# Kernel tuning notes

Measured on AMD Instinct MI355X. Metric: run time of the kernel, lower is better.

The kernel has to match this reference:

```python
import jax, jax.numpy as jnp
import numpy as np

V, H_BASE, D, L, K = 32000, 4096, 512, 2, 4
B = 64

def setup_inputs() -> dict:
    key = jax.random.key(0)
    ks = jax.random.split(key, 12)
    s = 0.02
    return {
        "hidden_state": jax.random.normal(ks[0], (B, H_BASE), jnp.float32),
        "in_proj_w": jax.random.normal(ks[1], (D, H_BASE), jnp.float32) * s,
        "in_proj_b": jnp.zeros((D,), jnp.float32),
        "w_ih0": jax.random.normal(ks[2], (3 * D, D), jnp.float32) * s,
        "w_hh0": jax.random.normal(ks[3], (3 * D, D), jnp.float32) * s,
        "b_ih0": jax.random.normal(ks[4], (3 * D,), jnp.float32) * s,
        "b_hh0": jax.random.normal(ks[5], (3 * D,), jnp.float32) * s,
        "w_ih1": jax.random.normal(ks[6], (3 * D, D), jnp.float32) * s,
        "w_hh1": jax.random.normal(ks[7], (3 * D, D), jnp.float32) * s,
        "b_ih1": jax.random.normal(ks[8], (3 * D,), jnp.float32) * s,
        "b_hh1": jax.random.normal(ks[9], (3 * D,), jnp.float32) * s,
        "embed": jax.random.normal(ks[10], (V, D), jnp.float32) * s,
        "out_w": jax.random.normal(ks[11], (V, D), jnp.float32) * s,
    }

def _gru_cell(x, h, w_ih, w_hh, b_ih, b_hh):
    # PyTorch GRU gate order: r, z, n
    gi = x @ w_ih.T + b_ih  # [B, 3D]
    gh = h @ w_hh.T + b_hh
    ir, iz, inn = jnp.split(gi, 3, axis=-1)
    hr, hz, hn = jnp.split(gh, 3, axis=-1)
    r = jax.nn.sigmoid(ir + hr)
    z = jax.nn.sigmoid(iz + hz)
    n = jnp.tanh(inn + r * hn)
    return (1.0 - z) * n + z * h

def reference(hidden_state, in_proj_w, in_proj_b, w_ih0, w_hh0, b_ih0, b_hh0,
              w_ih1, w_hh1, b_ih1, b_hh1, embed, out_w):
    b = hidden_state.shape[0]
    h0 = hidden_state @ in_proj_w.T + in_proj_b  # [B, D]
    h_l0 = h0
    h_l1 = h0
    x = jnp.zeros((b, in_proj_w.shape[0]), hidden_state.dtype)
    all_logits = []
    for _ in range(K):
        h_l0 = _gru_cell(x, h_l0, w_ih0, w_hh0, b_ih0, b_hh0)
        h_l1 = _gru_cell(h_l0, h_l1, w_ih1, w_hh1, b_ih1, b_hh1)
        logits = h_l1 @ out_w.T  # [B, V]
        all_logits.append(logits)
        x = embed[jnp.argmax(logits, axis=-1)]  # greedy next-token embed
    return jnp.stack(all_logits, axis=1)  # [B, K, V]
```

## Files before the change

### kernel.cpp

```cpp
#include <hip/hip_runtime.h>
#include <math.h>


typedef __attribute__((ext_vector_type(8))) short short8;
typedef __attribute__((ext_vector_type(4))) float f32x4;

__device__ __forceinline__ unsigned short f2bf_rne(float x) {
    unsigned u = __float_as_uint(x);
    unsigned r = (u + 0x7fffu + ((u >> 16) & 1u)) >> 16;
    return (unsigned short)r;
}
__device__ __forceinline__ void split2(float x, unsigned short& hi, unsigned short& lo) {
    unsigned u = __float_as_uint(x);
    hi = (unsigned short)(u >> 16);
    float r = x - __uint_as_float(u & 0xffff0000u);
    lo = f2bf_rne(r);
}

__device__ __forceinline__ void store_plane(unsigned short* hiP, unsigned short* loP,
                                            int m, int d, float v) {
    int s = d >> 6, cl = (d >> 3) & 7, e = d & 7;
    int off = m * 512 + s * 64 + ((cl ^ (m & 7)) * 8) + e;
    unsigned short hi, lo; split2(v, hi, lo);
    hiP[off] = hi; loP[off] = lo;
}

__device__ __forceinline__ void gload16(const void* g, void* lds) {
    __builtin_amdgcn_global_load_lds(
        (const __attribute__((address_space(1))) unsigned int*)g,
        (__attribute__((address_space(3))) unsigned int*)lds, 16, 0, 0);
}

__device__ __forceinline__ void split_w_body(
    const float* __restrict__ W, unsigned short* __restrict__ H,
    unsigned short* __restrict__ L, size_t g, int kclog)
{
    int n  = (int)(g >> kclog);
    int c8 = (int)g & ((1 << kclog) - 1);
    const float* src = W + g * 8;
    float4 v0 = *(const float4*)src;
    float4 v1 = *(const float4*)(src + 4);
    unsigned short h[8], l[8];
    split2(v0.x,h[0],l[0]); split2(v0.y,h[1],l[1]); split2(v0.z,h[2],l[2]); split2(v0.w,h[3],l[3]);
    split2(v1.x,h[4],l[4]); split2(v1.y,h[5],l[5]); split2(v1.z,h[6],l[6]); split2(v1.w,h[7],l[7]);
    uint4 ph = make_uint4((unsigned)h[0]|((unsigned)h[1]<<16), (unsigned)h[2]|((unsigned)h[3]<<16),
                          (unsigned)h[4]|((unsigned)h[5]<<16), (unsigned)h[6]|((unsigned)h[7]<<16));
    uint4 pl = make_uint4((unsigned)l[0]|((unsigned)l[1]<<16), (unsigned)l[2]|((unsigned)l[3]<<16),
                          (unsigned)l[4]|((unsigned)l[5]<<16), (unsigned)l[6]|((unsigned)l[7]<<16));
    int nt = n >> 7, row = n & 127;
    int ksi = c8 >> 3;
    int slot = (c8 & 7) ^ (row & 7);
    int tpr = 1 << (kclog - 3);
    size_t off = ((size_t)(nt * tpr + ksi) * 128 + row) * 64 + slot * 8;
    *(uint4*)(H + off) = ph;
    *(uint4*)(L + off) = pl;
}

__device__ __forceinline__ void split_a_body(
    const float* __restrict__ hidden, char* __restrict__ hidH,
    char* __restrict__ hidL, int g)
{
    int m = g >> 9;
    int cc = g & 511;
    int s = cc >> 3, cl = cc & 7;
    const float* src = hidden + m * 4096 + cc * 8;
    float4 v0 = *(const float4*)src;
    float4 v1 = *(const float4*)(src + 4);
    unsigned short h[8], l[8];
    split2(v0.x,h[0],l[0]); split2(v0.y,h[1],l[1]); split2(v0.z,h[2],l[2]); split2(v0.w,h[3],l[3]);
    split2(v1.x,h[4],l[4]); split2(v1.y,h[5],l[5]); split2(v1.z,h[6],l[6]); split2(v1.w,h[7],l[7]);
    uint4 ph = make_uint4((unsigned)h[0]|((unsigned)h[1]<<16), (unsigned)h[2]|((unsigned)h[3]<<16),
                          (unsigned)h[4]|((unsigned)h[5]<<16), (unsigned)h[6]|((unsigned)h[7]<<16));
    uint4 pl = make_uint4((unsigned)l[0]|((unsigned)l[1]<<16), (unsigned)l[2]|((unsigned)l[3]<<16),
                          (unsigned)l[4]|((unsigned)l[5]<<16), (unsigned)l[6]|((unsigned)l[7]<<16));
    int off = m * 8192 + s * 128 + ((cl ^ (m & 7)) * 16);
    *(uint4*)(hidH + off) = ph;
    *(uint4*)(hidL + off) = pl;
}

__device__ __forceinline__ void mfma_core(
    const unsigned short* __restrict__ AsH0, const unsigned short* __restrict__ AsL0,
    const unsigned short* __restrict__ BsH0, const unsigned short* __restrict__ BsL0,
    int wv, int lr, int lh, f32x4* acc)
{
#pragma unroll
    for (int kk2 = 0; kk2 < 2; ++kk2) {
        int aoff = lr * 64 + (((kk2 * 4 + lh) ^ (lr & 7)) * 8);
        short8 ah[4], al[4];
#pragma unroll
        for (int mt = 0; mt < 4; ++mt) {
            ah[mt] = *(const short8*)(AsH0 + mt * 1024 + aoff);
            al[mt] = *(const short8*)(AsL0 + mt * 1024 + aoff);
        }
        int brow = wv * 16 + lr;
        int boff = brow * 64 + (((kk2 * 4 + lh) ^ (brow & 7)) * 8);
        short8 bh = *(const short8*)(BsH0 + boff);
        short8 bl = *(const short8*)(BsL0 + boff);
#pragma unroll
        for (int mt = 0; mt < 4; ++mt) {
            acc[mt] = __builtin_amdgcn_mfma_f32_16x16x32_bf16(ah[mt], bh, acc[mt], 0, 0, 0);
            acc[mt] = __builtin_amdgcn_mfma_f32_16x16x32_bf16(ah[mt], bl, acc[mt], 0, 0, 0);
            acc[mt] = __builtin_amdgcn_mfma_f32_16x16x32_bf16(al[mt], bh, acc[mt], 0, 0, 0);
        }
    }
}

__device__ __forceinline__ void epilogue_write(
    float* __restrict__ C, int ldc, int n0, int wv, int lr, int lh, const f32x4* acc)
{
#pragma unroll
    for (int mt = 0; mt < 4; ++mt)
#pragma unroll
        for (int i = 0; i < 4; ++i) {
            int mm = mt * 16 + lh * 4 + i;
            C[mm * ldc + n0 + wv * 16 + lr] = acc[mt][i];
        }
}

template<bool ARGMAX>
__device__ __forceinline__ void mfma_gemm(
    const char* __restrict__ AH, const char* __restrict__ AL, int AstrideB, int akk0,
    const unsigned short* __restrict__ BH, const unsigned short* __restrict__ BL,
    size_t btileU, int nk,
    float* __restrict__ C, int ldc, int n0,
    unsigned short (*AsH)[4096], unsigned short (*AsL)[4096],
    unsigned short (*BsH)[8192], unsigned short (*BsL)[8192],
    float* __restrict__ pval, int* __restrict__ pidx, int bx)
{
    const int tid  = threadIdx.x;
    const int wv   = tid >> 6;
    const int lane = tid & 63;
    const int lr   = lane & 15;
    const int lh   = lane >> 4;
    const int m    = tid >> 3;
    const int cp   = tid & 7;

    f32x4 acc[4];
#pragma unroll
    for (int i = 0; i < 4; ++i) acc[i] = (f32x4){0.f, 0.f, 0.f, 0.f};

    auto stage = [&](int t, int p) {
        const int ka = (akk0 + t * 64) * 2;
        gload16(AH + m * AstrideB + ka + cp * 16, (char*)AsH[p] + wv * 1024);
        gload16(AL + m * AstrideB + ka + cp * 16, (char*)AsL[p] + wv * 1024);
        const char* bH = (const char*)BH + (btileU + (size_t)t * 8192) * 2;
        const char* bL = (const char*)BL + (btileU + (size_t)t * 8192) * 2;
        gload16(bH + wv * 2048 +        lane * 16, (char*)BsH[p] + wv * 2048);
        gload16(bH + wv * 2048 + 1024 + lane * 16, (char*)BsH[p] + wv * 2048 + 1024);
        gload16(bL + wv * 2048 +        lane * 16, (char*)BsL[p] + wv * 2048);
        gload16(bL + wv * 2048 + 1024 + lane * 16, (char*)BsL[p] + wv * 2048 + 1024);
    };

    stage(0, 0);
    __syncthreads();

    for (int t = 0; t < nk; ++t) {
        const int p = t & 1;
        if (t + 1 < nk) stage(t + 1, p ^ 1);
        mfma_core(AsH[p], AsL[p], BsH[p], BsL[p], wv, lr, lh, acc);
        __syncthreads();
    }

    epilogue_write(C, ldc, n0, wv, lr, lh, acc);

    if (ARGMAX) {
        float* sv = (float*)&AsH[0][0];
        int*   sc = (int*)&AsL[0][0];
#pragma unroll
        for (int mt = 0; mt < 4; ++mt)
#pragma unroll
            for (int i = 0; i < 4; ++i) {
                float v = acc[mt][i];
                int   c = n0 + wv * 16 + lr;
#pragma unroll
                for (int msk = 1; msk < 16; msk <<= 1) {
                    float ov = __shfl_xor(v, msk, 64);
                    int   oc = __shfl_xor(c, msk, 64);
                    if (ov > v || (ov == v && oc < c)) { v = ov; c = oc; }
                }
                if (lr == 0) {
                    int row = mt * 16 + lh * 4 + i;
                    sv[wv * 64 + row] = v;
                    sc[wv * 64 + row] = c;
                }
            }
        __syncthreads();
        if (tid < 64) {
            float v = sv[tid]; int c = sc[tid];
#pragma unroll
            for (int w = 1; w < 8; ++w) {
                float ov = sv[w * 64 + tid]; int oc = sc[w * 64 + tid];
                if (ov > v) { v = ov; c = oc; }
            }
            pval[bx * 64 + tid] = v;
            pidx[bx * 64 + tid] = c;
        }
    }
}

#define DECLARE_LDS() \
    __shared__ alignas(16) unsigned short AsH[2][4096]; \
    __shared__ alignas(16) unsigned short AsL[2][4096]; \
    __shared__ alignas(16) unsigned short BsH[2][8192]; \
    __shared__ alignas(16) unsigned short BsL[2][8192];

__global__ __launch_bounds__(512) void k_split_all(
    const float* __restrict__ out_w, const float* __restrict__ w_ih0,
    const float* __restrict__ w_hh0, const float* __restrict__ w_ih1,
    const float* __restrict__ w_hh1, const float* __restrict__ in_w,
    const float* __restrict__ hidden,
    unsigned short* __restrict__ owH, unsigned short* __restrict__ owL,
    unsigned short* __restrict__ gwH, unsigned short* __restrict__ gwL,
    unsigned short* __restrict__ inH, unsigned short* __restrict__ inL,
    char* __restrict__ hidH, char* __restrict__ hidL)
{
    size_t gt = (size_t)blockIdx.x * 512 + threadIdx.x;
    for (size_t u = gt; u < 2736128; u += 131072) {
        if (u < 2048000) {
            split_w_body(out_w, owH, owL, u, 6);
        } else if (u < 2441216) {
            size_t g = u - 2048000;
            int mat = (int)(g / 98304);
            const float* W = mat == 0 ? w_ih0 : mat == 1 ? w_hh0
                           : mat == 2 ? w_ih1 : w_hh1;
            split_w_body(W, gwH + (size_t)mat * 786432, gwL + (size_t)mat * 786432,
                         g % 98304, 6);
        } else if (u < 2703360) {
            split_w_body(in_w, inH, inL, u - 2441216, 9);
        } else {
            split_a_body(hidden, hidH, hidL, (int)(u - 2703360));
        }
    }
}

__global__ __launch_bounds__(512) void k_inproj(
    const char* __restrict__ hidH, const char* __restrict__ hidL,
    const unsigned short* __restrict__ inH, const unsigned short* __restrict__ inL,
    float* __restrict__ ipart)
{
    DECLARE_LDS();
    int nt = blockIdx.x & 3;
    int ks = blockIdx.x >> 2;
    mfma_gemm<false>(hidH, hidL, 8192, ks * 64,
                     inH, inL, (size_t)(nt * 64 + ks) * 8192, 1,
                     ipart + ks * 32768, 512, nt * 128,
                     AsH, AsL, BsH, BsL, nullptr, nullptr, 0);
}

__global__ __launch_bounds__(512) void k_reduce_inproj(
    const float* __restrict__ ipart, const float* __restrict__ bias,
    float* __restrict__ hA, float* __restrict__ hB,
    unsigned short* hAH, unsigned short* hAL,
    unsigned short* hBH, unsigned short* hBL)
{
    int i = blockIdx.x * 512 + threadIdx.x;
    int b = i >> 9;
    int d = i & 511;
    float s = bias[d];
#pragma unroll 8
    for (int ks = 0; ks < 64; ++ks) s += ipart[ks * 32768 + i];
    hA[i] = s;
    hB[i] = s;
    store_plane(hAH, hAL, b, d, s);
    store_plane(hBH, hBL, b, d, s);
}

__global__ __launch_bounds__(512) void k_gates3(
    int step,
    const float* __restrict__ pval, const int* __restrict__ pidx,
    const float* __restrict__ embed,
    const char* __restrict__ hAH, const char* __restrict__ hAL,
    const char* __restrict__ hBH, const char* __restrict__ hBL,
    const unsigned short* __restrict__ gwH, const unsigned short* __restrict__ gwL,
    float* __restrict__ gi0, float* __restrict__ gh0, float* __restrict__ gh1)
{
    DECLARE_LDS();
    const int bx  = blockIdx.x;
    const int tid = threadIdx.x;

    if (bx < 96) {
        int nt = bx % 12, ks = bx / 12;
        float* C = gi0 + ks * 98304;
        if (step == 0) {
            float4 z = make_float4(0.f, 0.f, 0.f, 0.f);
            for (int q = tid; q < 2048; q += 512) {
                int r = q >> 4, cq = q & 15;
                *(float4*)(C + r * 1536 + nt * 128 + cq * 4) = z;
            }
            return;
        }
        const int wv = tid >> 6, lane = tid & 63, lr = lane & 15, lh = lane >> 4;
        size_t btileU = ((size_t)nt * 8 + ks) * 8192;
        const char* bH = (const char*)gwH + btileU * 2;
        const char* bL = (const char*)gwL + btileU * 2;
        gload16(bH + wv * 2048 +        lane * 16, (char*)BsH[0] + wv * 2048);
        gload16(bH + wv * 2048 + 1024 + lane * 16, (char*)BsH[0] + wv * 2048 + 1024);
        gload16(bL + wv * 2048 +        lane * 16, (char*)BsL[0] + wv * 2048);
        gload16(bL + wv * 2048 + 1024 + lane * 16, (char*)BsL[0] + wv * 2048 + 1024);
        int r = tid >> 3, j0 = tid & 7;
        float v = -3.4e38f; int c = 0x7fffffff;
        for (int j = j0; j < 250; j += 8) {
            float ov = pval[j * 64 + r]; int oc = pidx[j * 64 + r];
            if (ov > v || (ov == v && oc < c)) { v = ov; c = oc; }
        }
#pragma unroll
        for (int msk = 1; msk < 8; msk <<= 1) {
            float ov = __shfl_xor(v, msk, 64);
            int   oc = __shfl_xor(c, msk, 64);
            if (ov > v || (ov == v && oc < c)) { v = ov; c = oc; }
        }
        int* stok = (int*)AsH[1];
        if (j0 == 0) stok[r] = c;
        __syncthreads();
        {
            int mm = tid >> 3, cp = tid & 7;
            int tok = stok[mm];
            const float* src = embed + (size_t)tok * 512 + ks * 64 + cp * 8;
            float4 v0 = *(const float4*)src;
            float4 v1 = *(const float4*)(src + 4);
            unsigned short h[8], l[8];
            split2(v0.x,h[0],l[0]); split2(v0.y,h[1],l[1]); split2(v0.z,h[2],l[2]); split2(v0.w,h[3],l[3]);
            split2(v1.x,h[4],l[4]); split2(v1.y,h[5],l[5]); split2(v1.z,h[6],l[6]); split2(v1.w,h[7],l[7]);
            uint4 ph = make_uint4((unsigned)h[0]|((unsigned)h[1]<<16), (unsigned)h[2]|((unsigned)h[3]<<16),
                                  (unsigned)h[4]|((unsigned)h[5]<<16), (unsigned)h[6]|((unsigned)h[7]<<16));
            uint4 pl = make_uint4((unsigned)l[0]|((unsigned)l[1]<<16), (unsigned)l[2]|((unsigned)l[3]<<16),
                                  (unsigned)l[4]|((unsigned)l[5]<<16), (unsigned)l[6]|((unsigned)l[7]<<16));
            int off = mm * 64 + ((cp ^ (mm & 7)) * 8);
            *(uint4*)(AsH[0] + off) = ph;
            *(uint4*)(AsL[0] + off) = pl;
        }
        __syncthreads();
        f32x4 acc[4];
#pragma unroll
        for (int i = 0; i < 4; ++i) acc[i] = (f32x4){0.f, 0.f, 0.f, 0.f};
        mfma_core(AsH[0], AsL[0], BsH[0], BsL[0], wv, lr, lh, acc);
        epilogue_write(C, 1536, nt * 128, wv, lr, lh, acc);
    } else if (bx < 192) {
        int idx = bx - 96;
        int nt = idx % 12, ks = idx / 12;
        size_t btile = ((size_t)96 + nt * 8 + ks) * 8192;
        mfma_gemm<false>((const char*)hAH, (const char*)hAL, 1024, ks * 64,
                         gwH, gwL, btile, 1,
                         gh0 + ks * 98304, 1536, nt * 128,
                         AsH, AsL, BsH, BsL, nullptr, nullptr, 0);
    } else {
        int idx = bx - 192;
        int nt = idx % 12, ks2 = idx / 12;
        size_t btile = ((size_t)288 + nt * 8 + ks2 * 2) * 8192;
        mfma_gemm<false>((const char*)hBH, (const char*)hBL, 1024, ks2 * 128,
                         gwH, gwL, btile, 2,
                         gh1 + ks2 * 98304, 1536, nt * 128,
                         AsH, AsL, BsH, BsL, nullptr, nullptr, 0);
    }
}

__global__ __launch_bounds__(512) void k_gates1(
    const char* __restrict__ hAH, const char* __restrict__ hAL,
    const unsigned short* __restrict__ gwH, const unsigned short* __restrict__ gwL,
    float* __restrict__ gi1)
{
    DECLARE_LDS();
    int nt = blockIdx.x % 12, ks = blockIdx.x / 12;
    size_t btile = ((size_t)192 + nt * 8 + ks) * 8192;
    mfma_gemm<false>((const char*)hAH, (const char*)hAL, 1024, ks * 64,
                     gwH, gwL, btile, 1,
                     gi1 + ks * 98304, 1536, nt * 128,
                     AsH, AsL, BsH, BsL, nullptr, nullptr, 0);
}

template<int NGI, int NGH>
__global__ __launch_bounds__(512) void k_combine(
    const float* __restrict__ gi, const float* __restrict__ gh,
    const float* __restrict__ b_ih, const float* __restrict__ b_hh,
    float* __restrict__ h, unsigned short* hH, unsigned short* hL)
{
    int i = blockIdx.x * 512 + threadIdx.x;
    int b = i >> 9;
    int d = i & 511;
    int base = b * 1536 + d;
    float ir = b_ih[d], iz = b_ih[d + 512], inn = b_ih[d + 1024];
    float hr = b_hh[d], hz = b_hh[d + 512], hn = b_hh[d + 1024];
#pragma unroll
    for (int ks = 0; ks < NGI; ++ks) {
        const float* g = gi + ks * 98304 + base;
        ir += g[0]; iz += g[512]; inn += g[1024];
    }
#pragma unroll
    for (int ks = 0; ks < NGH; ++ks) {
        const float* g = gh + ks * 98304 + base;
        hr += g[0]; hz += g[512]; hn += g[1024];
    }
    float r = 1.f / (1.f + expf(-(ir + hr)));
    float z = 1.f / (1.f + expf(-(iz + hz)));
    float n = tanhf(inn + r * hn);
    float hv = (1.f - z) * n + z * h[i];
    h[i] = hv;
    store_plane(hH, hL, b, d, hv);
}

__global__ __launch_bounds__(512) void k_logits(
    const char* __restrict__ hH, const char* __restrict__ hL,
    const unsigned short* __restrict__ WH, const unsigned short* __restrict__ WL,
    float* __restrict__ out, int step,
    float* __restrict__ pval, int* __restrict__ pidx)
{
    DECLARE_LDS();
    mfma_gemm<true>(hH, hL, 1024, 0,
                    WH, WL, (size_t)blockIdx.x * 8 * 8192, 8,
                    out + step * 32000, 128000, blockIdx.x * 128,
                    AsH, AsL, BsH, BsL, pval, pidx, blockIdx.x);
}

extern "C" void kernel_launch(void* const* d_in, const int* in_sizes, int n_in,
                              void* d_out, int out_size, void* d_ws, size_t ws_size,
                              hipStream_t stream)
{
    const float* hidden = (const float*)d_in[0];
    const float* in_w   = (const float*)d_in[1];
    const float* in_b   = (const float*)d_in[2];
    const float* w_ih0  = (const float*)d_in[3];
    const float* w_hh0  = (const float*)d_in[4];
    const float* b_ih0  = (const float*)d_in[5];
    const float* b_hh0  = (const float*)d_in[6];
    const float* w_ih1  = (const float*)d_in[7];
    const float* w_hh1  = (const float*)d_in[8];
    const float* b_ih1  = (const float*)d_in[9];
    const float* b_hh1  = (const float*)d_in[10];
    const float* embed  = (const float*)d_in[11];
    const float* out_w  = (const float*)d_in[12];
    float* out = (float*)d_out;
    char*  ws  = (char*)d_ws;

    float* hA  = (float*)(ws + 0);
    float* hB  = (float*)(ws + 131072);
    unsigned short* hAH = (unsigned short*)(ws + 262144);
    unsigned short* hAL = (unsigned short*)(ws + 327680);
    unsigned short* hBH = (unsigned short*)(ws + 393216);
    unsigned short* hBL = (unsigned short*)(ws + 458752);
    char* hidH = ws + 524288;
    char* hidL = ws + 1048576;
    float* g_gi0 = (float*)(ws + 1572864);
    float* g_gh0 = (float*)(ws + 4718592);
    float* g_gi1 = (float*)(ws + 7864320);
    float* g_gh1 = (float*)(ws + 11010048);
    float* pval  = (float*)(ws + 12582912);
    int*   pidx  = (int*)  (ws + 12648448);
    float* ipart = (float*)(ws + 12713984);
    unsigned short* owH = (unsigned short*)(ws + 21102592);
    unsigned short* owL = (unsigned short*)(ws + 53870592);
    unsigned short* gwH = (unsigned short*)(ws + 86638592);
    unsigned short* gwL = (unsigned short*)(ws + 92930048);
    unsigned short* inH = (unsigned short*)(ws + 99221504);
    unsigned short* inL = (unsigned short*)(ws + 103415808);

    k_split_all<<<256, 512, 0, stream>>>(out_w, w_ih0, w_hh0, w_ih1, w_hh1,
                                         in_w, hidden,
                                         owH, owL, gwH, gwL, inH, inL, hidH, hidL);
    k_inproj<<<256, 512, 0, stream>>>(hidH, hidL, inH, inL, ipart);
    k_reduce_inproj<<<64, 512, 0, stream>>>(ipart, in_b, hA, hB,
                                            hAH, hAL, hBH, hBL);

    for (int step = 0; step < 4; ++step) {
        k_gates3<<<240, 512, 0, stream>>>(step, pval, pidx, embed,
                                          (char*)hAH, (char*)hAL,
                                          (char*)hBH, (char*)hBL,
                                          gwH, gwL, g_gi0, g_gh0, g_gh1);
        k_combine<8, 8><<<64, 512, 0, stream>>>(g_gi0, g_gh0, b_ih0, b_hh0,
                                                hA, hAH, hAL);
        k_gates1<<<96, 512, 0, stream>>>((char*)hAH, (char*)hAL, gwH, gwL, g_gi1);
        k_combine<8, 4><<<64, 512, 0, stream>>>(g_gi1, g_gh1, b_ih1, b_hh1,
                                                hB, hBH, hBL);
        k_logits<<<250, 512, 0, stream>>>((char*)hBH, (char*)hBL, owH, owL,
                                          out, step, pval, pidx);
    }
}
```

Measured before the change: 370.4 us.

## Restructure GRU step pipeline: fuse combine into GEMMs, atomic argmax, hoist hidden-gate GEMMs

The per-step kernel sequence is reorganised. The layer-0 gate combine is fused into a kernel that also computes the layer-1 input gates and the next step's layer-0 hidden gates, using double-buffered h and gh0. The layer-1 hidden-gate GEMM for the next step now shares a launch with the logits GEMM. The per-block argmax partials plus a separate reduction are replaced by a packed 64-bit atomicMax. The split kernel launch shape also changes. Together these aim to cut kernel launches and global round-trips per step, at the cost of redundant combine work across column tiles and extra atomic traffic.

```diff
diff --git a/kernel.cpp b/kernel.cpp
--- a/kernel.cpp
+++ b/kernel.cpp
@@ -117,6 +117,11 @@
         }
 }
 
+__device__ __forceinline__ unsigned orderable(float v) {
+    unsigned u = __float_as_uint(v);
+    return (u & 0x80000000u) ? ~u : (u | 0x80000000u);
+}
+
 template<bool ARGMAX>
 __device__ __forceinline__ void mfma_gemm(
     const char* __restrict__ AH, const char* __restrict__ AL, int AstrideB, int akk0,
@@ -125,7 +130,7 @@
     float* __restrict__ C, int ldc, int n0,
     unsigned short (*AsH)[4096], unsigned short (*AsL)[4096],
     unsigned short (*BsH)[8192], unsigned short (*BsL)[8192],
-    float* __restrict__ pval, int* __restrict__ pidx, int bx)
+    unsigned long long* __restrict__ packed)
 {
     const int tid  = threadIdx.x;
     const int wv   = tid >> 6;
@@ -190,10 +195,11 @@
 #pragma unroll
             for (int w = 1; w < 8; ++w) {
                 float ov = sv[w * 64 + tid]; int oc = sc[w * 64 + tid];
-                if (ov > v) { v = ov; c = oc; }
+                if (ov > v || (ov == v && oc < c)) { v = ov; c = oc; }
             }
-            pval[bx * 64 + tid] = v;
-            pidx[bx * 64 + tid] = c;
+            unsigned long long pk =
+                ((unsigned long long)orderable(v) << 32) | (unsigned)(~(unsigned)c);
+            atomicMax(packed + tid, pk);
         }
     }
 }
@@ -204,7 +210,7 @@
     __shared__ alignas(16) unsigned short BsH[2][8192]; \
     __shared__ alignas(16) unsigned short BsL[2][8192];
 
-__global__ __launch_bounds__(512) void k_split_all(
+__global__ __launch_bounds__(256) void k_split_all(
     const float* __restrict__ out_w, const float* __restrict__ w_ih0,
     const float* __restrict__ w_hh0, const float* __restrict__ w_ih1,
     const float* __restrict__ w_hh1, const float* __restrict__ in_w,
@@ -214,8 +220,8 @@
     unsigned short* __restrict__ inH, unsigned short* __restrict__ inL,
     char* __restrict__ hidH, char* __restrict__ hidL)
 {
-    size_t gt = (size_t)blockIdx.x * 512 + threadIdx.x;
-    for (size_t u = gt; u < 2736128; u += 131072) {
+    size_t gt = (size_t)blockIdx.x * 256 + threadIdx.x;
+    for (size_t u = gt; u < 2736128; u += 524288) {
         if (u < 2048000) {
             split_w_body(out_w, owH, owL, u, 6);
         } else if (u < 2441216) {
@@ -244,12 +250,12 @@
     mfma_gemm<false>(hidH, hidL, 8192, ks * 64,
                      inH, inL, (size_t)(nt * 64 + ks) * 8192, 1,
                      ipart + ks * 32768, 512, nt * 128,
-                     AsH, AsL, BsH, BsL, nullptr, nullptr, 0);
+                     AsH, AsL, BsH, BsL, nullptr);
 }
 
 __global__ __launch_bounds__(512) void k_reduce_inproj(
     const float* __restrict__ ipart, const float* __restrict__ bias,
-    float* __restrict__ hA, float* __restrict__ hB,
+    float* __restrict__ hA0, float* __restrict__ hB,
     unsigned short* hAH, unsigned short* hAL,
     unsigned short* hBH, unsigned short* hBL)
 {
@@ -259,120 +265,191 @@
     float s = bias[d];
 #pragma unroll 8
     for (int ks = 0; ks < 64; ++ks) s += ipart[ks * 32768 + i];
-    hA[i] = s;
+    hA0[i] = s;
     hB[i] = s;
     store_plane(hAH, hAL, b, d, s);
     store_plane(hBH, hBL, b, d, s);
 }
 
-__global__ __launch_bounds__(512) void k_gates3(
-    int step,
-    const float* __restrict__ pval, const int* __restrict__ pidx,
-    const float* __restrict__ embed,
+__global__ __launch_bounds__(512) void k_gh_init(
     const char* __restrict__ hAH, const char* __restrict__ hAL,
     const char* __restrict__ hBH, const char* __restrict__ hBL,
     const unsigned short* __restrict__ gwH, const unsigned short* __restrict__ gwL,
-    float* __restrict__ gi0, float* __restrict__ gh0, float* __restrict__ gh1)
+    float* __restrict__ gh0_b0, float* __restrict__ gh1)
 {
     DECLARE_LDS();
-    const int bx  = blockIdx.x;
-    const int tid = threadIdx.x;
-
+    int bx = blockIdx.x;
     if (bx < 96) {
         int nt = bx % 12, ks = bx / 12;
-        float* C = gi0 + ks * 98304;
-        if (step == 0) {
-            float4 z = make_float4(0.f, 0.f, 0.f, 0.f);
-            for (int q = tid; q < 2048; q += 512) {
-                int r = q >> 4, cq = q & 15;
-                *(float4*)(C + r * 1536 + nt * 128 + cq * 4) = z;
-            }
-            return;
-        }
-        const int wv = tid >> 6, lane = tid & 63, lr = lane & 15, lh = lane >> 4;
-        size_t btileU = ((size_t)nt * 8 + ks) * 8192;
-        const char* bH = (const char*)gwH + btileU * 2;
-        const char* bL = (const char*)gwL + btileU * 2;
-        gload16(bH + wv * 2048 +        lane * 16, (char*)BsH[0] + wv * 2048);
-        gload16(bH + wv * 2048 + 1024 + lane * 16, (char*)BsH[0] + wv * 2048 + 1024);
-        gload16(bL + wv * 2048 +        lane * 16, (char*)BsL[0] + wv * 2048);
-        gload16(bL + wv * 2048 + 1024 + lane * 16, (char*)BsL[0] + wv * 2048 + 1024);
-        int r = tid >> 3, j0 = tid & 7;
-        float v = -3.4e38f; int c = 0x7fffffff;
-        for (int j = j0; j < 250; j += 8) {
-            float ov = pval[j * 64 + r]; int oc = pidx[j * 64 + r];
-            if (ov > v || (ov == v && oc < c)) { v = ov; c = oc; }
-        }
-#pragma unroll
-        for (int msk = 1; msk < 8; msk <<= 1) {
-            float ov = __shfl_xor(v, msk, 64);
-            int   oc = __shfl_xor(c, msk, 64);
-            if (ov > v || (ov == v && oc < c)) { v = ov; c = oc; }
-        }
-        int* stok = (int*)AsH[1];
-        if (j0 == 0) stok[r] = c;
-        __syncthreads();
-        {
-            int mm = tid >> 3, cp = tid & 7;
-            int tok = stok[mm];
-            const float* src = embed + (size_t)tok * 512 + ks * 64 + cp * 8;
-            float4 v0 = *(const float4*)src;
-            float4 v1 = *(const float4*)(src + 4);
-            unsigned short h[8], l[8];
-            split2(v0.x,h[0],l[0]); split2(v0.y,h[1],l[1]); split2(v0.z,h[2],l[2]); split2(v0.w,h[3],l[3]);
-            split2(v1.x,h[4],l[4]); split2(v1.y,h[5],l[5]); split2(v1.z,h[6],l[6]); split2(v1.w,h[7],l[7]);
-            uint4 ph = make_uint4((unsigned)h[0]|((unsigned)h[1]<<16), (unsigned)h[2]|((unsigned)h[3]<<16),
-                                  (unsigned)h[4]|((unsigned)h[5]<<16), (unsigned)h[6]|((unsigned)h[7]<<16));
-            uint4 pl = make_uint4((unsigned)l[0]|((unsigned)l[1]<<16), (unsigned)l[2]|((unsigned)l[3]<<16),
-                                  (unsigned)l[4]|((unsigned)l[5]<<16), (unsigned)l[6]|((unsigned)l[7]<<16));
-            int off = mm * 64 + ((cp ^ (mm & 7)) * 8);
-            *(uint4*)(AsH[0] + off) = ph;
-            *(uint4*)(AsL[0] + off) = pl;
-        }
-        __syncthreads();
-        f32x4 acc[4];
-#pragma unroll
-        for (int i = 0; i < 4; ++i) acc[i] = (f32x4){0.f, 0.f, 0.f, 0.f};
-        mfma_core(AsH[0], AsL[0], BsH[0], BsL[0], wv, lr, lh, acc);
-        epilogue_write(C, 1536, nt * 128, wv, lr, lh, acc);
-    } else if (bx < 192) {
+        size_t btile = ((size_t)96 + nt * 8 + ks) * 8192;
+        mfma_gemm<false>(hAH, hAL, 1024, ks * 64, gwH, gwL, btile, 1,
+                         gh0_b0 + ks * 98304, 1536, nt * 128,
+                         AsH, AsL, BsH, BsL, nullptr);
+    } else {
         int idx = bx - 96;
-        int nt = idx % 12, ks = idx / 12;
-        size_t btile = ((size_t)96 + nt * 8 + ks) * 8192;
-        mfma_gemm<false>((const char*)hAH, (const char*)hAL, 1024, ks * 64,
-                         gwH, gwL, btile, 1,
-                         gh0 + ks * 98304, 1536, nt * 128,
-                         AsH, AsL, BsH, BsL, nullptr, nullptr, 0);
-    } else {
-        int idx = bx - 192;
         int nt = idx % 12, ks2 = idx / 12;
         size_t btile = ((size_t)288 + nt * 8 + ks2 * 2) * 8192;
-        mfma_gemm<false>((const char*)hBH, (const char*)hBL, 1024, ks2 * 128,
-                         gwH, gwL, btile, 2,
+        mfma_gemm<false>(hBH, hBL, 1024, ks2 * 128, gwH, gwL, btile, 2,
                          gh1 + ks2 * 98304, 1536, nt * 128,
-                         AsH, AsL, BsH, BsL, nullptr, nullptr, 0);
-    }
-}
-
-__global__ __launch_bounds__(512) void k_gates1(
-    const char* __restrict__ hAH, const char* __restrict__ hAL,
+                         AsH, AsL, BsH, BsL, nullptr);
+    }
+}
+
+__global__ __launch_bounds__(512) void k_gi0(
+    const unsigned long long* __restrict__ packed,
+    const float* __restrict__ embed,
     const unsigned short* __restrict__ gwH, const unsigned short* __restrict__ gwL,
-    float* __restrict__ gi1)
+    float* __restrict__ gi0)
 {
     DECLARE_LDS();
+    const int tid = threadIdx.x;
+    const int wv = tid >> 6, lane = tid & 63, lr = lane & 15, lh = lane >> 4;
     int nt = blockIdx.x % 12, ks = blockIdx.x / 12;
-    size_t btile = ((size_t)192 + nt * 8 + ks) * 8192;
-    mfma_gemm<false>((const char*)hAH, (const char*)hAL, 1024, ks * 64,
-                     gwH, gwL, btile, 1,
-                     gi1 + ks * 98304, 1536, nt * 128,
-                     AsH, AsL, BsH, BsL, nullptr, nullptr, 0);
-}
-
-template<int NGI, int NGH>
-__global__ __launch_bounds__(512) void k_combine(
-    const float* __restrict__ gi, const float* __restrict__ gh,
+
+    size_t btileU = ((size_t)nt * 8 + ks) * 8192;
+    const char* bH = (const char*)gwH + btileU * 2;
+    const char* bL = (const char*)gwL + btileU * 2;
+    gload16(bH + wv * 2048 +        lane * 16, (char*)BsH[0] + wv * 2048);
+    gload16(bH + wv * 2048 + 1024 + lane * 16, (char*)BsH[0] + wv * 2048 + 1024);
+    gload16(bL + wv * 2048 +        lane * 16, (char*)BsL[0] + wv * 2048);
+    gload16(bL + wv * 2048 + 1024 + lane * 16, (char*)BsL[0] + wv * 2048 + 1024);
+
+    {
+        int mm = tid >> 3, cp = tid & 7;
+        unsigned long long pk = packed[mm];
+        int tok = (int)(~(unsigned)(pk & 0xffffffffu));
+        const float* src = embed + (size_t)tok * 512 + ks * 64 + cp * 8;
+        float4 v0 = *(const float4*)src;
+        float4 v1 = *(const float4*)(src + 4);
+        unsigned short h[8], l[8];
+        split2(v0.x,h[0],l[0]); split2(v0.y,h[1],l[1]); split2(v0.z,h[2],l[2]); split2(v0.w,h[3],l[3]);
+        split2(v1.x,h[4],l[4]); split2(v1.y,h[5],l[5]); split2(v1.z,h[6],l[6]); split2(v1.w,h[7],l[7]);
+        uint4 ph = make_uint4((unsigned)h[0]|((unsigned)h[1]<<16), (unsigned)h[2]|((unsigned)h[3]<<16),
+                              (unsigned)h[4]|((unsigned)h[5]<<16), (unsigned)h[6]|((unsigned)h[7]<<16));
+        uint4 pl = make_uint4((unsigned)l[0]|((unsigned)l[1]<<16), (unsigned)l[2]|((unsigned)l[3]<<16),
+                              (unsigned)l[4]|((unsigned)l[5]<<16), (unsigned)l[6]|((unsigned)l[7]<<16));
+        int off = mm * 64 + ((cp ^ (mm & 7)) * 8);
+        *(uint4*)(AsH[0] + off) = ph;
+        *(uint4*)(AsL[0] + off) = pl;
+    }
+    __syncthreads();
+
+    f32x4 acc[4];
+#pragma unroll
+    for (int i = 0; i < 4; ++i) acc[i] = (f32x4){0.f, 0.f, 0.f, 0.f};
+    mfma_core(AsH[0], AsL[0], BsH[0], BsL[0], wv, lr, lh, acc);
+    epilogue_write(gi0 + ks * 98304, 1536, nt * 128, wv, lr, lh, acc);
+}
+
+__global__ __launch_bounds__(512) void k_fused_l1(
+    int step,
+    const float* __restrict__ hA_cur, float* __restrict__ hA_nxt,
+    const float* __restrict__ gi0,
+    const float* __restrict__ gh0_cur, float* __restrict__ gh0_nxt,
+    float* __restrict__ gi1,
+    const unsigned short* __restrict__ gwH, const unsigned short* __restrict__ gwL,
+    const float* __restrict__ b_ih0, const float* __restrict__ b_hh0)
+{
+    DECLARE_LDS();
+    const int bx = blockIdx.x, tid = threadIdx.x;
+    const int nt = bx % 12, ks = (bx / 12) & 7, mat = bx / 96;
+    if (mat == 1 && step == 3) return;
+    const int wv = tid >> 6, lane = tid & 63, lr = lane & 15, lh = lane >> 4;
+
+    size_t btileU = ((size_t)(mat ? 96 : 192) + nt * 8 + ks) * 8192;
+    const char* bH = (const char*)gwH + btileU * 2;
+    const char* bL = (const char*)gwL + btileU * 2;
+    gload16(bH + wv * 2048 +        lane * 16, (char*)BsH[0] + wv * 2048);
+    gload16(bH + wv * 2048 + 1024 + lane * 16, (char*)BsH[0] + wv * 2048 + 1024);
+    gload16(bL + wv * 2048 +        lane * 16, (char*)BsL[0] + wv * 2048);
+    gload16(bL + wv * 2048 + 1024 + lane * 16, (char*)BsL[0] + wv * 2048 + 1024);
+
+    {
+        const int b = tid >> 3, cl = tid & 7;
+        const int d0 = ks * 64 + cl * 8;
+        float ir[8], iz[8], in_[8], hr[8], hz[8], hn[8];
+        {
+            float4 u0, u1;
+            u0 = *(const float4*)(b_ih0 + d0);        u1 = *(const float4*)(b_ih0 + d0 + 4);
+            ir[0]=u0.x; ir[1]=u0.y; ir[2]=u0.z; ir[3]=u0.w; ir[4]=u1.x; ir[5]=u1.y; ir[6]=u1.z; ir[7]=u1.w;
+            u0 = *(const float4*)(b_ih0 + 512 + d0);  u1 = *(const float4*)(b_ih0 + 512 + d0 + 4);
+            iz[0]=u0.x; iz[1]=u0.y; iz[2]=u0.z; iz[3]=u0.w; iz[4]=u1.x; iz[5]=u1.y; iz[6]=u1.z; iz[7]=u1.w;
+            u0 = *(const float4*)(b_ih0 + 1024 + d0); u1 = *(const float4*)(b_ih0 + 1024 + d0 + 4);
+            in_[0]=u0.x; in_[1]=u0.y; in_[2]=u0.z; in_[3]=u0.w; in_[4]=u1.x; in_[5]=u1.y; in_[6]=u1.z; in_[7]=u1.w;
+            u0 = *(const float4*)(b_hh0 + d0);        u1 = *(const float4*)(b_hh0 + d0 + 4);
+            hr[0]=u0.x; hr[1]=u0.y; hr[2]=u0.z; hr[3]=u0.w; hr[4]=u1.x; hr[5]=u1.y; hr[6]=u1.z; hr[7]=u1.w;
+            u0 = *(const float4*)(b_hh0 + 512 + d0);  u1 = *(const float4*)(b_hh0 + 512 + d0 + 4);
+            hz[0]=u0.x; hz[1]=u0.y; hz[2]=u0.z; hz[3]=u0.w; hz[4]=u1.x; hz[5]=u1.y; hz[6]=u1.z; hz[7]=u1.w;
+            u0 = *(const float4*)(b_hh0 + 1024 + d0); u1 = *(const float4*)(b_hh0 + 1024 + d0 + 4);
+            hn[0]=u0.x; hn[1]=u0.y; hn[2]=u0.z; hn[3]=u0.w; hn[4]=u1.x; hn[5]=u1.y; hn[6]=u1.z; hn[7]=u1.w;
+        }
+        if (step > 0) {
+#pragma unroll
+            for (int p = 0; p < 8; ++p) {
+                const float* g = gi0 + p * 98304 + b * 1536 + d0;
+                float4 a0, a1;
+                a0 = *(const float4*)(g);        a1 = *(const float4*)(g + 4);
+                ir[0]+=a0.x; ir[1]+=a0.y; ir[2]+=a0.z; ir[3]+=a0.w; ir[4]+=a1.x; ir[5]+=a1.y; ir[6]+=a1.z; ir[7]+=a1.w;
+                a0 = *(const float4*)(g + 512);  a1 = *(const float4*)(g + 516);
+                iz[0]+=a0.x; iz[1]+=a0.y; iz[2]+=a0.z; iz[3]+=a0.w; iz[4]+=a1.x; iz[5]+=a1.y; iz[6]+=a1.z; iz[7]+=a1.w;
+                a0 = *(const float4*)(g + 1024); a1 = *(const float4*)(g + 1028);
+                in_[0]+=a0.x; in_[1]+=a0.y; in_[2]+=a0.z; in_[3]+=a0.w; in_[4]+=a1.x; in_[5]+=a1.y; in_[6]+=a1.z; in_[7]+=a1.w;
+            }
+        }
+#pragma unroll
+        for (int p = 0; p < 8; ++p) {
+            const float* g = gh0_cur + p * 98304 + b * 1536 + d0;
+            float4 a0, a1;
+            a0 = *(const float4*)(g);        a1 = *(const float4*)(g + 4);
+            hr[0]+=a0.x; hr[1]+=a0.y; hr[2]+=a0.z; hr[3]+=a0.w; hr[4]+=a1.x; hr[5]+=a1.y; hr[6]+=a1.z; hr[7]+=a1.w;
+            a0 = *(const float4*)(g + 512);  a1 = *(const float4*)(g + 516);
+            hz[0]+=a0.x; hz[1]+=a0.y; hz[2]+=a0.z; hz[3]+=a0.w; hz[4]+=a1.x; hz[5]+=a1.y; hz[6]+=a1.z; hz[7]+=a1.w;
+            a0 = *(const float4*)(g + 1024); a1 = *(const float4*)(g + 1028);
+            hn[0]+=a0.x; hn[1]+=a0.y; hn[2]+=a0.z; hn[3]+=a0.w; hn[4]+=a1.x; hn[5]+=a1.y; hn[6]+=a1.z; hn[7]+=a1.w;
+        }
+        float hold[8];
+        {
+            float4 u0 = *(const float4*)(hA_cur + b * 512 + d0);
+            float4 u1 = *(const float4*)(hA_cur + b * 512 + d0 + 4);
+            hold[0]=u0.x; hold[1]=u0.y; hold[2]=u0.z; hold[3]=u0.w;
+            hold[4]=u1.x; hold[5]=u1.y; hold[6]=u1.z; hold[7]=u1.w;
+        }
+        float hv[8];
+        unsigned short hh[8], ll[8];
+#pragma unroll
+        for (int e = 0; e < 8; ++e) {
+            float r = 1.f / (1.f + expf(-(ir[e] + hr[e])));
+            float z = 1.f / (1.f + expf(-(iz[e] + hz[e])));
+            float n = tanhf(in_[e] + r * hn[e]);
+            hv[e] = (1.f - z) * n + z * hold[e];
+            split2(hv[e], hh[e], ll[e]);
+        }
+        uint4 ph = make_uint4((unsigned)hh[0]|((unsigned)hh[1]<<16), (unsigned)hh[2]|((unsigned)hh[3]<<16),
+                              (unsigned)hh[4]|((unsigned)hh[5]<<16), (unsigned)hh[6]|((unsigned)hh[7]<<16));
+        uint4 pl = make_uint4((unsigned)ll[0]|((unsigned)ll[1]<<16), (unsigned)ll[2]|((unsigned)ll[3]<<16),
+                              (unsigned)ll[4]|((unsigned)ll[5]<<16), (unsigned)ll[6]|((unsigned)ll[7]<<16));
+        int off = b * 64 + ((cl ^ (b & 7)) * 8);
+        *(uint4*)(AsH[0] + off) = ph;
+        *(uint4*)(AsL[0] + off) = pl;
+        if (mat == 0 && nt == 0) {
+            *(float4*)(hA_nxt + b * 512 + d0)     = make_float4(hv[0], hv[1], hv[2], hv[3]);
+            *(float4*)(hA_nxt + b * 512 + d0 + 4) = make_float4(hv[4], hv[5], hv[6], hv[7]);
+        }
+    }
+    __syncthreads();
+
+    f32x4 acc[4];
+#pragma unroll
+    for (int i = 0; i < 4; ++i) acc[i] = (f32x4){0.f, 0.f, 0.f, 0.f};
+    mfma_core(AsH[0], AsL[0], BsH[0], BsL[0], wv, lr, lh, acc);
+    epilogue_write((mat ? gh0_nxt : gi1) + ks * 98304, 1536, nt * 128, wv, lr, lh, acc);
+}
+
+__global__ __launch_bounds__(512) void k_combine1(
+    const float* __restrict__ gi1, const float* __restrict__ gh1,
     const float* __restrict__ b_ih, const float* __restrict__ b_hh,
-    float* __restrict__ h, unsigned short* hH, unsigned short* hL)
+    float* __restrict__ hB, unsigned short* hBH, unsigned short* hBL,
+    unsigned long long* __restrict__ packed)
 {
     int i = blockIdx.x * 512 + threadIdx.x;
     int b = i >> 9;
@@ -381,34 +458,46 @@
     float ir = b_ih[d], iz = b_ih[d + 512], inn = b_ih[d + 1024];
     float hr = b_hh[d], hz = b_hh[d + 512], hn = b_hh[d + 1024];
 #pragma unroll
-    for (int ks = 0; ks < NGI; ++ks) {
-        const float* g = gi + ks * 98304 + base;
+    for (int ks = 0; ks < 8; ++ks) {
+        const float* g = gi1 + ks * 98304 + base;
         ir += g[0]; iz += g[512]; inn += g[1024];
     }
 #pragma unroll
-    for (int ks = 0; ks < NGH; ++ks) {
-        const float* g = gh + ks * 98304 + base;
+    for (int ks = 0; ks < 4; ++ks) {
+        const float* g = gh1 + ks * 98304 + base;
         hr += g[0]; hz += g[512]; hn += g[1024];
     }
     float r = 1.f / (1.f + expf(-(ir + hr)));
     float z = 1.f / (1.f + expf(-(iz + hz)));
     float n = tanhf(inn + r * hn);
-    float hv = (1.f - z) * n + z * h[i];
-    h[i] = hv;
-    store_plane(hH, hL, b, d, hv);
-}
-
-__global__ __launch_bounds__(512) void k_logits(
-    const char* __restrict__ hH, const char* __restrict__ hL,
-    const unsigned short* __restrict__ WH, const unsigned short* __restrict__ WL,
+    float hv = (1.f - z) * n + z * hB[i];
+    hB[i] = hv;
+    store_plane(hBH, hBL, b, d, hv);
+    if (blockIdx.x == 0 && threadIdx.x < 64) packed[threadIdx.x] = 0ull;
+}
+
+__global__ __launch_bounds__(512) void k_logits_gh1(
+    const char* __restrict__ hBH, const char* __restrict__ hBL,
+    const unsigned short* __restrict__ owH, const unsigned short* __restrict__ owL,
+    const unsigned short* __restrict__ gwH, const unsigned short* __restrict__ gwL,
     float* __restrict__ out, int step,
-    float* __restrict__ pval, int* __restrict__ pidx)
+    unsigned long long* __restrict__ packed, float* __restrict__ gh1)
 {
     DECLARE_LDS();
-    mfma_gemm<true>(hH, hL, 1024, 0,
-                    WH, WL, (size_t)blockIdx.x * 8 * 8192, 8,
-                    out + step * 32000, 128000, blockIdx.x * 128,
-                    AsH, AsL, BsH, BsL, pval, pidx, blockIdx.x);
+    int bx = blockIdx.x;
+    if (bx < 48) {
+        if (step == 3) return;
+        int nt = bx % 12, ks2 = bx / 12;
+        size_t btile = ((size_t)288 + nt * 8 + ks2 * 2) * 8192;
+        mfma_gemm<false>(hBH, hBL, 1024, ks2 * 128, gwH, gwL, btile, 2,
+                         gh1 + ks2 * 98304, 1536, nt * 128,
+                         AsH, AsL, BsH, BsL, nullptr);
+    } else {
+        int lx = bx - 48;
+        mfma_gemm<true>(hBH, hBL, 1024, 0, owH, owL, (size_t)lx * 8 * 8192, 8,
+                        out + step * 32000, 128000, lx * 128,
+                        AsH, AsL, BsH, BsL, packed);
+    }
 }
 
 extern "C" void kernel_launch(void* const* d_in, const int* in_sizes, int n_in,
@@ -431,46 +520,53 @@
     float* out = (float*)d_out;
     char*  ws  = (char*)d_ws;
 
-    float* hA  = (float*)(ws + 0);
-    float* hB  = (float*)(ws + 131072);
-    unsigned short* hAH = (unsigned short*)(ws + 262144);
-    unsigned short* hAL = (unsigned short*)(ws + 327680);
-    unsigned short* hBH = (unsigned short*)(ws + 393216);
-    unsigned short* hBL = (unsigned short*)(ws + 458752);
-    char* hidH = ws + 524288;
-    char* hidL = ws + 1048576;
-    float* g_gi0 = (float*)(ws + 1572864);
-    float* g_gh0 = (float*)(ws + 4718592);
-    float* g_gi1 = (float*)(ws + 7864320);
-    float* g_gh1 = (float*)(ws + 11010048);
-    float* pval  = (float*)(ws + 12582912);
-    int*   pidx  = (int*)  (ws + 12648448);
-    float* ipart = (float*)(ws + 12713984);
-    unsigned short* owH = (unsigned short*)(ws + 21102592);
-    unsigned short* owL = (unsigned short*)(ws + 53870592);
-    unsigned short* gwH = (unsigned short*)(ws + 86638592);
-    unsigned short* gwL = (unsigned short*)(ws + 92930048);
-    unsigned short* inH = (unsigned short*)(ws + 99221504);
-    unsigned short* inL = (unsigned short*)(ws + 103415808);
-
-    k_split_all<<<256, 512, 0, stream>>>(out_w, w_ih0, w_hh0, w_ih1, w_hh1,
-                                         in_w, hidden,
-                                         owH, owL, gwH, gwL, inH, inL, hidH, hidL);
+    float* hA0 = (float*)(ws + 0);
+    float* hA1 = (float*)(ws + 131072);
+    float* hB  = (float*)(ws + 262144);
+    unsigned short* hAH = (unsigned short*)(ws + 393216);
+    unsigned short* hAL = (unsigned short*)(ws + 458752);
+    unsigned short* hBH = (unsigned short*)(ws + 524288);
+    unsigned short* hBL = (unsigned short*)(ws + 589824);
+    char* hidH = ws + 655360;
+    char* hidL = ws + 1179648;
+    float* gi0    = (float*)(ws + 1703936);
+    float* gh0b0  = (float*)(ws + 4849664);
+    float* gh0b1  = (float*)(ws + 7995392);
+    float* gi1    = (float*)(ws + 11141120);
+    float* gh1    = (float*)(ws + 14286848);
+    unsigned long long* packed = (unsigned long long*)(ws + 15859712);
+    float* ipart  = (float*)(ws + 15863808);
+    unsigned short* owH = (unsigned short*)(ws + 24252416);
+    unsigned short* owL = (unsigned short*)(ws + 57020416);
+    unsigned short* gwH = (unsigned short*)(ws + 89788416);
+    unsigned short* gwL = (unsigned short*)(ws + 96079872);
+    unsigned short* inH = (unsigned short*)(ws + 102371328);
+    unsigned short* inL = (unsigned short*)(ws + 106565632);
+
+    k_split_all<<<2048, 256, 0, stream>>>(out_w, w_ih0, w_hh0, w_ih1, w_hh1,
+                                          in_w, hidden,
+                                          owH, owL, gwH, gwL, inH, inL, hidH, hidL);
     k_inproj<<<256, 512, 0, stream>>>(hidH, hidL, inH, inL, ipart);
-    k_reduce_inproj<<<64, 512, 0, stream>>>(ipart, in_b, hA, hB,
+    k_reduce_inproj<<<64, 512, 0, stream>>>(ipart, in_b, hA0, hB,
                                             hAH, hAL, hBH, hBL);
-
+    k_gh_init<<<144, 512, 0, stream>>>((char*)hAH, (char*)hAL,
+                                       (char*)hBH, (char*)hBL,
+                                       gwH, gwL, gh0b0, gh1);
+
+    float* hA_bufs[2] = { hA0, hA1 };
+    float* gh0_bufs[2] = { gh0b0, gh0b1 };
     for (int step = 0; step < 4; ++step) {
-        k_gates3<<<240, 512, 0, stream>>>(step, pval, pidx, embed,
-                                          (char*)hAH, (char*)hAL,
-                                          (char*)hBH, (char*)hBL,
-                                          gwH, gwL, g_gi0, g_gh0, g_gh1);
-        k_combine<8, 8><<<64, 512, 0, stream>>>(g_gi0, g_gh0, b_ih0, b_hh0,
-                                                hA, hAH, hAL);
-        k_gates1<<<96, 512, 0, stream>>>((char*)hAH, (char*)hAL, gwH, gwL, g_gi1);
-        k_combine<8, 4><<<64, 512, 0, stream>>>(g_gi1, g_gh1, b_ih1, b_hh1,
-                                                hB, hBH, hBL);
-        k_logits<<<250, 512, 0, stream>>>((char*)hBH, (char*)hBL, owH, owL,
-                                          out, step, pval, pidx);
-    }
-}
+        if (step > 0)
+            k_gi0<<<96, 512, 0, stream>>>(packed, embed, gwH, gwL, gi0);
+        k_fused_l1<<<192, 512, 0, stream>>>(step,
+                                            hA_bufs[step & 1], hA_bufs[(step + 1) & 1],
+                                            gi0,
+                                            gh0_bufs[step & 1], gh0_bufs[(step + 1) & 1],
+                                            gi1, gwH, gwL, b_ih0, b_hh0);
+        k_combine1<<<64, 512, 0, stream>>>(gi1, gh1, b_ih1, b_hh1,
+                                           hB, hBH, hBL, packed);
+        k_logits_gh1<<<298, 512, 0, stream>>>((char*)hBH, (char*)hBL,
+                                              owH, owL, gwH, gwL,
+                                              out, step, packed, gh1);
+    }
+}
```

After: 399.3 us. 7.8% more time.
